# Optimization experiments

Measured on AMD Instinct MI355X. Metric: run time of the kernel, lower is better.

## Reference

```python
import jax, jax.numpy as jnp
import numpy as np

RES_W, RES_H = 256, 256
MAX_SAMPLES = 384
TF_RES = 128
FOV_DEG = 30.0
NEAR, FAR = 0.1, 100.0
BG = 0.0
HIT_EPS = 1e-3


def _normalize(v, axis=-1):
    return v / jnp.linalg.norm(v, axis=axis, keepdims=True)


def trilinear_sample(vol, tex):
    # vol: [X,Y,Z], tex: [...,3] in voxel coordinates
    res = np.array(vol.shape, dtype=np.float32)
    p = jnp.clip(tex, 0.0, jnp.asarray(res - 1.0 - 1e-6, jnp.float32))
    lo = jnp.floor(p).astype(jnp.int32)
    f = p - lo.astype(p.dtype)
    hi = jnp.minimum(lo + 1, jnp.asarray(res.astype(np.int32) - 1))
    x0, y0, z0 = lo[..., 0], lo[..., 1], lo[..., 2]
    x1, y1, z1 = hi[..., 0], hi[..., 1], hi[..., 2]
    fx, fy, fz = f[..., 0], f[..., 1], f[..., 2]
    c000 = vol[x0, y0, z0]; c100 = vol[x1, y0, z0]
    c010 = vol[x0, y1, z0]; c110 = vol[x1, y1, z0]
    c001 = vol[x0, y0, z1]; c101 = vol[x1, y0, z1]
    c011 = vol[x0, y1, z1]; c111 = vol[x1, y1, z1]
    c00 = c000 * (1 - fx) + c100 * fx
    c10 = c010 * (1 - fx) + c110 * fx
    c01 = c001 * (1 - fx) + c101 * fx
    c11 = c011 * (1 - fx) + c111 * fx
    c0 = c00 * (1 - fy) + c10 * fy
    c1 = c01 * (1 - fy) + c11 * fy
    return c0 * (1 - fz) + c1 * fz


def tf_lookup(tf, x):
    # tf: [T,4], x: [...] intensity in [0,1]
    T = tf.shape[0]
    xi = jnp.clip(x, 0.0, 1.0) * (T - 1)
    lo = jnp.floor(xi).astype(jnp.int32)
    hi = jnp.minimum(lo + 1, T - 1)
    f = (xi - lo.astype(xi.dtype))[..., None]
    return tf[lo] * (1 - f) + tf[hi] * f


def render_one(vol, tf, cam, sr):
    # vol [X,Y,Z], tf [T,4], cam [3] -> [W,H,5] (rgba + depth)
    W, H = RES_W, RES_H
    fwd = _normalize(-cam)
    world_up = jnp.array([0.0, 1.0, 0.0], jnp.float32)
    right = _normalize(jnp.cross(fwd, world_up))
    up = jnp.cross(right, fwd)
    tanf = jnp.tan(jnp.float32(np.radians(FOV_DEG) / 2))
    aspect = W / H
    u = ((jnp.arange(W) + 0.5) / W * 2 - 1) * tanf * aspect  # [W]
    v = ((jnp.arange(H) + 0.5) / H * 2 - 1) * tanf           # [H]
    dirs = fwd + u[:, None, None] * right + v[None, :, None] * up  # [W,H,3]
    dirs = _normalize(dirs)
    # ray-box intersection against [-1,1]^3
    inv = 1.0 / dirs
    t_lo = (-1.0 - cam) * inv
    t_hi = (1.0 - cam) * inv
    tmin = jnp.max(jnp.minimum(t_lo, t_hi), axis=-1)
    tmax = jnp.min(jnp.maximum(t_lo, t_hi), axis=-1)
    hit = (tmax >= 0.0) & (tmin <= tmax)
    entry = jnp.maximum(tmin, NEAR)
    dist = jnp.where(hit, jnp.maximum(tmax - entry, 0.0), 0.0)
    vol_max = max(vol.shape)
    # Nyquist: step = voxel size (2/vol_max) / sampling_rate
    ns = jnp.clip(jnp.ceil(dist * 0.5 * vol_max * sr), 1.0, MAX_SAMPLES)
    step = dist / ns
    k = jnp.arange(MAX_SAMPLES, dtype=jnp.float32)
    t = entry[..., None] + (k + 0.5) * step[..., None]            # [W,H,S]
    valid = (k < ns[..., None]) & hit[..., None]
    pos = cam + t[..., None] * dirs[..., None, :]                 # [W,H,S,3]
    res_m1 = jnp.asarray(np.array(vol.shape, np.float32) - 1.0)
    tex = (pos * 0.5 + 0.5) * res_m1
    intensity = trilinear_sample(vol, tex)                        # [W,H,S]
    rgba = tf_lookup(tf, intensity)                               # [W,H,S,4]
    a = rgba[..., 3]
    a = 1.0 - (1.0 - a) ** (1.0 / sr)   # opacity correction for sampling rate
    a = jnp.where(valid, a, 0.0)
    one_m = 1.0 - a
    cp = jnp.cumprod(one_m, axis=-1)
    T_excl = jnp.concatenate([jnp.ones_like(cp[..., :1]), cp[..., :-1]], axis=-1)
    w = T_excl * a                                                # [W,H,S]
    rgb = jnp.einsum('whs,whsc->whc', w, rgba[..., :3])
    acc = jnp.sum(w, axis=-1)
    rgb_out = rgb + (1.0 - acc)[..., None] * BG
    # FirstHitDepth
    hit_s = a > HIT_EPS
    any_hit = jnp.any(hit_s, axis=-1)
    first = jnp.argmax(hit_s, axis=-1)
    t_first = jnp.take_along_axis(t, first[..., None], axis=-1)[..., 0]
    depth = jnp.where(any_hit, (t_first - NEAR) / (FAR - NEAR), 1.0)
    return jnp.concatenate([rgb_out, acc[..., None], depth[..., None]], axis=-1)


def setup_inputs() -> dict:
    key = jax.random.key(0)
    k1, k2, k3 = jax.random.split(key, 3)
    volume = jax.random.uniform(k1, (1, 256, 256, 256), dtype=jnp.float32)
    tf = jax.random.uniform(k2, (1, TF_RES, 4), dtype=jnp.float32)
    look_from = jnp.array([[0.9, 0.7, -2.2]], jnp.float32) + 0.1 * jax.random.normal(k3, (1, 3), dtype=jnp.float32)
    return {"volume": volume, "tf": tf, "look_from": look_from, "sampling_rate": 1}


def reference(volume, tf, look_from, sampling_rate):
    sr = float(sampling_rate)
    return jax.vmap(lambda v, t, c: render_one(v, t, c, sr))(volume, tf, look_from)
```

## Files before the change

### kernel.cpp

```cpp
#include <hip/hip_runtime.h>
#include <math.h>

#define RES_W 256
#define RES_H 256
#define MAX_SAMPLES 384
#define TF_RES 128

__global__ __launch_bounds__(64) void raycast_kernel(
    const float* __restrict__ vol,
    const float* __restrict__ tf,
    const float* __restrict__ cam_p,
    const int*   __restrict__ sr_p,
    float* __restrict__ out)
{
    #pragma clang fp contract(off)

    __shared__ float4 tf_s[TF_RES];
    const int tid = threadIdx.y * 8 + threadIdx.x;
    const float4* tf4 = (const float4*)tf;
    tf_s[tid]      = tf4[tid];
    tf_s[tid + 64] = tf4[tid + 64];
    __syncthreads();

    const int h = blockIdx.x * 8 + threadIdx.x;
    const int w = blockIdx.y * 8 + threadIdx.y;

    const float cx = cam_p[0], cy = cam_p[1], cz = cam_p[2];
    const int   sr_i = sr_p[0];
    const float srf = (float)sr_i;

    float nx = -cx, ny = -cy, nz = -cz;
    float fl = __fsqrt_rn((nx*nx + ny*ny) + nz*nz);
    float fx = nx / fl, fy = ny / fl, fz = nz / fl;
    float rxu = 0.0f - fz;
    float rzu = fx;
    float rl = __fsqrt_rn((rxu*rxu + 0.0f) + rzu*rzu);
    float rx = rxu / rl, rz = rzu / rl;
    float ux = 0.0f - rz*fy;
    float uy = rz*fx - rx*fz;
    float uz = rx*fy;

    const float ang32 = (float)((30.0 * 0.017453292519943295) * 0.5);
    const float tan_half = (float)tan((double)ang32);

    float uu = ((((float)w + 0.5f) / 256.0f) * 2.0f - 1.0f) * tan_half;
    float vv = ((((float)h + 0.5f) / 256.0f) * 2.0f - 1.0f) * tan_half;

    float dx = (fx + uu*rx) + vv*ux;
    float dy = (fy + 0.0f ) + vv*uy;
    float dz = (fz + uu*rz) + vv*uz;
    float dl = __fsqrt_rn((dx*dx + dy*dy) + dz*dz);
    dx = dx / dl; dy = dy / dl; dz = dz / dl;

    float ivx = 1.0f/dx, ivy = 1.0f/dy, ivz = 1.0f/dz;
    float tlx = (-1.0f - cx)*ivx, thx = (1.0f - cx)*ivx;
    float tly = (-1.0f - cy)*ivy, thy = (1.0f - cy)*ivy;
    float tlz = (-1.0f - cz)*ivz, thz = (1.0f - cz)*ivz;
    float tmin = fmaxf(fmaxf(fminf(tlx,thx), fminf(tly,thy)), fminf(tlz,thz));
    float tmax = fminf(fminf(fmaxf(tlx,thx), fmaxf(tly,thy)), fmaxf(tlz,thz));
    bool hit = (tmax >= 0.0f) && (tmin <= tmax);

    float entry = fmaxf(tmin, 0.1f);
    float dist  = hit ? fmaxf(tmax - entry, 0.0f) : 0.0f;
    float nsf   = fminf(fmaxf(ceilf(((dist * 0.5f) * 256.0f) * srf), 1.0f), 384.0f);
    int   ns    = (int)nsf;
    float step  = dist / nsf;

    float rgb_r = 0.0f, rgb_g = 0.0f, rgb_b = 0.0f;
    float acc = 0.0f;
    float Texcl = 1.0f;
    float depth = 1.0f;
    bool  found = false;

    if (hit) {
        for (int k = 0; k < ns; ++k) {
            float t  = entry + ((float)k + 0.5f) * step;
            float px = (cx + t*dx);
            float py = (cy + t*dy);
            float pz = (cz + t*dz);
            px = ((px * 0.5f) + 0.5f) * 255.0f;
            py = ((py * 0.5f) + 0.5f) * 255.0f;
            pz = ((pz * 0.5f) + 0.5f) * 255.0f;
            px = fminf(fmaxf(px, 0.0f), 255.0f);
            py = fminf(fmaxf(py, 0.0f), 255.0f);
            pz = fminf(fmaxf(pz, 0.0f), 255.0f);
            int x0 = (int)floorf(px), y0 = (int)floorf(py), z0 = (int)floorf(pz);
            float ffx = px - (float)x0;
            float ffy = py - (float)y0;
            float ffz = pz - (float)z0;
            int x1 = min(x0 + 1, 255);
            int y1 = min(y0 + 1, 255);
            int z1 = min(z0 + 1, 255);

            int bx0 = x0 << 16, bx1 = x1 << 16;
            int by0 = y0 << 8,  by1 = y1 << 8;
            float c000 = vol[bx0 + by0 + z0];
            float c100 = vol[bx1 + by0 + z0];
            float c010 = vol[bx0 + by1 + z0];
            float c110 = vol[bx1 + by1 + z0];
            float c001 = vol[bx0 + by0 + z1];
            float c101 = vol[bx1 + by0 + z1];
            float c011 = vol[bx0 + by1 + z1];
            float c111 = vol[bx1 + by1 + z1];

            float omx = 1.0f - ffx, omy = 1.0f - ffy, omz = 1.0f - ffz;
            float c00 = c000*omx + c100*ffx;
            float c10 = c010*omx + c110*ffx;
            float c01 = c001*omx + c101*ffx;
            float c11 = c011*omx + c111*ffx;
            float c0  = c00*omy + c10*ffy;
            float c1  = c01*omy + c11*ffy;
            float intensity = c0*omz + c1*ffz;

            float xi = fminf(fmaxf(intensity, 0.0f), 1.0f) * 127.0f;
            int lo  = (int)floorf(xi);
            int hi2 = min(lo + 1, 127);
            float tfr = xi - (float)lo;
            float omt = 1.0f - tfr;
            float4 ca = tf_s[lo];
            float4 cb = tf_s[hi2];
            float cr  = ca.x*omt + cb.x*tfr;
            float cg  = ca.y*omt + cb.y*tfr;
            float cbb = ca.z*omt + cb.z*tfr;
            float a   = ca.w*omt + cb.w*tfr;

            if (sr_i == 1) {
                a = 1.0f - (1.0f - a);
            } else {
                a = 1.0f - powf(1.0f - a, 1.0f / srf);
            }

            float one_m = 1.0f - a;
            float wgt = Texcl * a;
            rgb_r += wgt * cr;
            rgb_g += wgt * cg;
            rgb_b += wgt * cbb;
            acc   += wgt;
            if (!found && a > 1e-3f) {
                found = true;
                depth = (t - 0.1f) / 99.9f;
            }
            Texcl = Texcl * one_m;
            if (found && Texcl < 1e-7f) break;
        }
    }

    {
        int oi = (w * RES_H + h) * 5;
        out[oi + 0] = rgb_r;
        out[oi + 1] = rgb_g;
        out[oi + 2] = rgb_b;
        out[oi + 3] = acc;
        out[oi + 4] = depth;
    }
}

extern "C" void kernel_launch(void* const* d_in, const int* in_sizes, int n_in,
                              void* d_out, int out_size, void* d_ws, size_t ws_size,
                              hipStream_t stream) {
    const float* vol = (const float*)d_in[0];
    const float* tf  = (const float*)d_in[1];
    const float* cam = (const float*)d_in[2];
    const int*   sr  = (const int*)d_in[3];
    float* out = (float*)d_out;

    dim3 block(8, 8, 1);
    dim3 grid(RES_H / 8, RES_W / 8, 1);
    raycast_kernel<<<grid, block, 0, stream>>>(vol, tf, cam, sr, out);
}
```

Baseline: 117.0 us.

## Batch four ray samples per iteration and remap block order across XCDs

The sample loop now computes positions and issues the gathers for four samples up front, then interpolates all four and composites them in order. This exposes more independent memory loads per thread to hide gather latency, at the cost of more registers and up to three wasted samples after early termination. The launch becomes a 1D grid whose block index is permuted so that spatially adjacent tiles land on the same chiplet, aiming to improve L2 locality for the volume reads.

```diff
diff --git a/kernel.cpp b/kernel.cpp
--- a/kernel.cpp
+++ b/kernel.cpp
@@ -16,14 +16,18 @@
     #pragma clang fp contract(off)
 
     __shared__ float4 tf_s[TF_RES];
-    const int tid = threadIdx.y * 8 + threadIdx.x;
+    const int tid = (int)threadIdx.x;
     const float4* tf4 = (const float4*)tf;
     tf_s[tid]      = tf4[tid];
     tf_s[tid + 64] = tf4[tid + 64];
     __syncthreads();
 
-    const int h = blockIdx.x * 8 + threadIdx.x;
-    const int w = blockIdx.y * 8 + threadIdx.y;
+    const int b    = (int)blockIdx.x;
+    const int tile = (b % 8) * 128 + (b / 8);
+    const int tile_h = tile % 32;
+    const int tile_w = tile / 32;
+    const int h = tile_h * 8 + (tid % 8);
+    const int w = tile_w * 8 + (tid / 8);
 
     const float cx = cam_p[0], cy = cam_p[1], cz = cam_p[2];
     const int   sr_i = sr_p[0];
@@ -73,74 +77,85 @@
     bool  found = false;
 
     if (hit) {
-        for (int k = 0; k < ns; ++k) {
-            float t  = entry + ((float)k + 0.5f) * step;
-            float px = (cx + t*dx);
-            float py = (cy + t*dy);
-            float pz = (cz + t*dz);
-            px = ((px * 0.5f) + 0.5f) * 255.0f;
-            py = ((py * 0.5f) + 0.5f) * 255.0f;
-            pz = ((pz * 0.5f) + 0.5f) * 255.0f;
-            px = fminf(fmaxf(px, 0.0f), 255.0f);
-            py = fminf(fmaxf(py, 0.0f), 255.0f);
-            pz = fminf(fmaxf(pz, 0.0f), 255.0f);
-            int x0 = (int)floorf(px), y0 = (int)floorf(py), z0 = (int)floorf(pz);
-            float ffx = px - (float)x0;
-            float ffy = py - (float)y0;
-            float ffz = pz - (float)z0;
-            int x1 = min(x0 + 1, 255);
-            int y1 = min(y0 + 1, 255);
-            int z1 = min(z0 + 1, 255);
-
-            int bx0 = x0 << 16, bx1 = x1 << 16;
-            int by0 = y0 << 8,  by1 = y1 << 8;
-            float c000 = vol[bx0 + by0 + z0];
-            float c100 = vol[bx1 + by0 + z0];
-            float c010 = vol[bx0 + by1 + z0];
-            float c110 = vol[bx1 + by1 + z0];
-            float c001 = vol[bx0 + by0 + z1];
-            float c101 = vol[bx1 + by0 + z1];
-            float c011 = vol[bx0 + by1 + z1];
-            float c111 = vol[bx1 + by1 + z1];
-
-            float omx = 1.0f - ffx, omy = 1.0f - ffy, omz = 1.0f - ffz;
-            float c00 = c000*omx + c100*ffx;
-            float c10 = c010*omx + c110*ffx;
-            float c01 = c001*omx + c101*ffx;
-            float c11 = c011*omx + c111*ffx;
-            float c0  = c00*omy + c10*ffy;
-            float c1  = c01*omy + c11*ffy;
-            float intensity = c0*omz + c1*ffz;
-
-            float xi = fminf(fmaxf(intensity, 0.0f), 1.0f) * 127.0f;
-            int lo  = (int)floorf(xi);
-            int hi2 = min(lo + 1, 127);
-            float tfr = xi - (float)lo;
-            float omt = 1.0f - tfr;
-            float4 ca = tf_s[lo];
-            float4 cb = tf_s[hi2];
-            float cr  = ca.x*omt + cb.x*tfr;
-            float cg  = ca.y*omt + cb.y*tfr;
-            float cbb = ca.z*omt + cb.z*tfr;
-            float a   = ca.w*omt + cb.w*tfr;
-
-            if (sr_i == 1) {
-                a = 1.0f - (1.0f - a);
-            } else {
-                a = 1.0f - powf(1.0f - a, 1.0f / srf);
+        for (int k0 = 0; k0 < ns; k0 += 4) {
+            float t_[4], val[4][8], ffx_[4], ffy_[4], ffz_[4];
+            #pragma unroll
+            for (int j = 0; j < 4; ++j) {
+                float t  = entry + ((float)(k0 + j) + 0.5f) * step;
+                t_[j] = t;
+                float px = (cx + t*dx);
+                float py = (cy + t*dy);
+                float pz = (cz + t*dz);
+                px = ((px * 0.5f) + 0.5f) * 255.0f;
+                py = ((py * 0.5f) + 0.5f) * 255.0f;
+                pz = ((pz * 0.5f) + 0.5f) * 255.0f;
+                px = fminf(fmaxf(px, 0.0f), 255.0f);
+                py = fminf(fmaxf(py, 0.0f), 255.0f);
+                pz = fminf(fmaxf(pz, 0.0f), 255.0f);
+                int x0 = (int)floorf(px), y0 = (int)floorf(py), z0 = (int)floorf(pz);
+                ffx_[j] = px - (float)x0;
+                ffy_[j] = py - (float)y0;
+                ffz_[j] = pz - (float)z0;
+                int x1 = min(x0 + 1, 255);
+                int y1 = min(y0 + 1, 255);
+                int z1 = min(z0 + 1, 255);
+                int bx0 = x0 << 16, bx1 = x1 << 16;
+                int by0 = y0 << 8,  by1 = y1 << 8;
+                val[j][0] = vol[bx0 + by0 + z0];
+                val[j][1] = vol[bx1 + by0 + z0];
+                val[j][2] = vol[bx0 + by1 + z0];
+                val[j][3] = vol[bx1 + by1 + z0];
+                val[j][4] = vol[bx0 + by0 + z1];
+                val[j][5] = vol[bx1 + by0 + z1];
+                val[j][6] = vol[bx0 + by1 + z1];
+                val[j][7] = vol[bx1 + by1 + z1];
             }
-
-            float one_m = 1.0f - a;
-            float wgt = Texcl * a;
-            rgb_r += wgt * cr;
-            rgb_g += wgt * cg;
-            rgb_b += wgt * cbb;
-            acc   += wgt;
-            if (!found && a > 1e-3f) {
-                found = true;
-                depth = (t - 0.1f) / 99.9f;
+            float tfr_[4];
+            float4 ca_[4], cb_[4];
+            #pragma unroll
+            for (int j = 0; j < 4; ++j) {
+                float omx = 1.0f - ffx_[j], omy = 1.0f - ffy_[j], omz = 1.0f - ffz_[j];
+                float c00 = val[j][0]*omx + val[j][1]*ffx_[j];
+                float c10 = val[j][2]*omx + val[j][3]*ffx_[j];
+                float c01 = val[j][4]*omx + val[j][5]*ffx_[j];
+                float c11 = val[j][6]*omx + val[j][7]*ffx_[j];
+                float c0  = c00*omy + c10*ffy_[j];
+                float c1  = c01*omy + c11*ffy_[j];
+                float intensity = c0*omz + c1*ffz_[j];
+                float xi = fminf(fmaxf(intensity, 0.0f), 1.0f) * 127.0f;
+                int lo  = (int)floorf(xi);
+                int hi2 = min(lo + 1, 127);
+                tfr_[j] = xi - (float)lo;
+                ca_[j] = tf_s[lo];
+                cb_[j] = tf_s[hi2];
             }
-            Texcl = Texcl * one_m;
+            #pragma unroll
+            for (int j = 0; j < 4; ++j) {
+                if (k0 + j < ns) {
+                    float tfr = tfr_[j];
+                    float omt = 1.0f - tfr;
+                    float cr  = ca_[j].x*omt + cb_[j].x*tfr;
+                    float cg  = ca_[j].y*omt + cb_[j].y*tfr;
+                    float cbb = ca_[j].z*omt + cb_[j].z*tfr;
+                    float a   = ca_[j].w*omt + cb_[j].w*tfr;
+                    if (sr_i == 1) {
+                        a = 1.0f - (1.0f - a);
+                    } else {
+                        a = 1.0f - powf(1.0f - a, 1.0f / srf);
+                    }
+                    float one_m = 1.0f - a;
+                    float wgt = Texcl * a;
+                    rgb_r += wgt * cr;
+                    rgb_g += wgt * cg;
+                    rgb_b += wgt * cbb;
+                    acc   += wgt;
+                    if (!found && a > 1e-3f) {
+                        found = true;
+                        depth = (t_[j] - 0.1f) / 99.9f;
+                    }
+                    Texcl = Texcl * one_m;
+                }
+            }
             if (found && Texcl < 1e-7f) break;
         }
     }
@@ -164,7 +179,5 @@
     const int*   sr  = (const int*)d_in[3];
     float* out = (float*)d_out;
 
-    dim3 block(8, 8, 1);
-    dim3 grid(RES_H / 8, RES_W / 8, 1);
-    raycast_kernel<<<grid, block, 0, stream>>>(vol, tf, cam, sr, out);
+    raycast_kernel<<<dim3(1024), dim3(64), 0, stream>>>(vol, tf, cam, sr, out);
 }
```

After: 113.0 us. -3.4%, faster.

## Parallelize each ray across 32 lanes with scan-based compositing

Applied to the files above, without the earlier changes.

Each ray is now handled by 32 lanes that sample 32 consecutive steps at once. Transmittance comes from a warp shuffle prefix product, colour and alpha from shuffle reductions, and first-hit depth from a min-reduction. The transfer function moves to a structure-of-arrays layout in shared memory, and blocks are remapped with a swizzle. This exposes far more memory-level parallelism for the scattered volume fetches than one-thread-per-ray marching, at the cost of shuffle overhead, wasted samples past early termination within a 32-chunk, and slightly different float summation order.

```diff
diff --git a/kernel.cpp b/kernel.cpp
--- a/kernel.cpp
+++ b/kernel.cpp
@@ -3,10 +3,9 @@
 
 #define RES_W 256
 #define RES_H 256
-#define MAX_SAMPLES 384
 #define TF_RES 128
 
-__global__ __launch_bounds__(64) void raycast_kernel(
+__global__ __launch_bounds__(256, 8) void raycast_kernel(
     const float* __restrict__ vol,
     const float* __restrict__ tf,
     const float* __restrict__ cam_p,
@@ -15,15 +14,22 @@
 {
     #pragma clang fp contract(off)
 
-    __shared__ float4 tf_s[TF_RES];
-    const int tid = threadIdx.y * 8 + threadIdx.x;
-    const float4* tf4 = (const float4*)tf;
-    tf_s[tid]      = tf4[tid];
-    tf_s[tid + 64] = tf4[tid + 64];
+    __shared__ float tfR[TF_RES], tfG[TF_RES], tfB[TF_RES], tfA[TF_RES];
+    const int tid = (int)threadIdx.x;
+    if (tid < TF_RES) {
+        float4 e = ((const float4*)tf)[tid];
+        tfR[tid] = e.x; tfG[tid] = e.y; tfB[tid] = e.z; tfA[tid] = e.w;
+    }
     __syncthreads();
 
-    const int h = blockIdx.x * 8 + threadIdx.x;
-    const int w = blockIdx.y * 8 + threadIdx.y;
+    const int lane = tid & 63;
+    const int sub  = lane & 31;
+
+    const int b  = (int)blockIdx.x;
+    const int sb = (b & 7) * 1024 + (b >> 3);
+    const int ray = sb * 8 + (tid >> 5);
+    const int h = ray & 255;
+    const int w = ray >> 8;
 
     const float cx = cam_p[0], cy = cam_p[1], cz = cam_p[2];
     const int   sr_i = sr_p[0];
@@ -66,86 +72,108 @@
     int   ns    = (int)nsf;
     float step  = dist / nsf;
 
-    float rgb_r = 0.0f, rgb_g = 0.0f, rgb_b = 0.0f;
-    float acc = 0.0f;
-    float Texcl = 1.0f;
+    float rgb_r = 0.0f, rgb_g = 0.0f, rgb_b = 0.0f, acc = 0.0f;
+    float T_prev = 1.0f;
     float depth = 1.0f;
     bool  found = false;
 
-    if (hit) {
-        for (int k = 0; k < ns; ++k) {
-            float t  = entry + ((float)k + 0.5f) * step;
-            float px = (cx + t*dx);
-            float py = (cy + t*dy);
-            float pz = (cz + t*dz);
-            px = ((px * 0.5f) + 0.5f) * 255.0f;
-            py = ((py * 0.5f) + 0.5f) * 255.0f;
-            pz = ((pz * 0.5f) + 0.5f) * 255.0f;
-            px = fminf(fmaxf(px, 0.0f), 255.0f);
-            py = fminf(fmaxf(py, 0.0f), 255.0f);
-            pz = fminf(fmaxf(pz, 0.0f), 255.0f);
-            int x0 = (int)floorf(px), y0 = (int)floorf(py), z0 = (int)floorf(pz);
-            float ffx = px - (float)x0;
-            float ffy = py - (float)y0;
-            float ffz = pz - (float)z0;
-            int x1 = min(x0 + 1, 255);
-            int y1 = min(y0 + 1, 255);
-            int z1 = min(z0 + 1, 255);
+    for (int base = 0; ; ) {
+        const int  k     = base + sub;
+        const bool valid = hit && (k < ns);
 
-            int bx0 = x0 << 16, bx1 = x1 << 16;
-            int by0 = y0 << 8,  by1 = y1 << 8;
-            float c000 = vol[bx0 + by0 + z0];
-            float c100 = vol[bx1 + by0 + z0];
-            float c010 = vol[bx0 + by1 + z0];
-            float c110 = vol[bx1 + by1 + z0];
-            float c001 = vol[bx0 + by0 + z1];
-            float c101 = vol[bx1 + by0 + z1];
-            float c011 = vol[bx0 + by1 + z1];
-            float c111 = vol[bx1 + by1 + z1];
+        float t  = entry + ((float)k + 0.5f) * step;
+        float px = (cx + t*dx);
+        float py = (cy + t*dy);
+        float pz = (cz + t*dz);
+        px = ((px * 0.5f) + 0.5f) * 255.0f;
+        py = ((py * 0.5f) + 0.5f) * 255.0f;
+        pz = ((pz * 0.5f) + 0.5f) * 255.0f;
+        px = fminf(fmaxf(px, 0.0f), 255.0f);
+        py = fminf(fmaxf(py, 0.0f), 255.0f);
+        pz = fminf(fmaxf(pz, 0.0f), 255.0f);
+        int x0 = (int)floorf(px), y0 = (int)floorf(py), z0 = (int)floorf(pz);
+        float ffx = px - (float)x0;
+        float ffy = py - (float)y0;
+        float ffz = pz - (float)z0;
+        int x1 = min(x0 + 1, 255);
+        int y1 = min(y0 + 1, 255);
+        int z1 = min(z0 + 1, 255);
+        int bx0 = x0 << 16, bx1 = x1 << 16;
+        int by0 = y0 << 8,  by1 = y1 << 8;
+        float c000 = vol[bx0 + by0 + z0];
+        float c100 = vol[bx1 + by0 + z0];
+        float c010 = vol[bx0 + by1 + z0];
+        float c110 = vol[bx1 + by1 + z0];
+        float c001 = vol[bx0 + by0 + z1];
+        float c101 = vol[bx1 + by0 + z1];
+        float c011 = vol[bx0 + by1 + z1];
+        float c111 = vol[bx1 + by1 + z1];
 
-            float omx = 1.0f - ffx, omy = 1.0f - ffy, omz = 1.0f - ffz;
-            float c00 = c000*omx + c100*ffx;
-            float c10 = c010*omx + c110*ffx;
-            float c01 = c001*omx + c101*ffx;
-            float c11 = c011*omx + c111*ffx;
-            float c0  = c00*omy + c10*ffy;
-            float c1  = c01*omy + c11*ffy;
-            float intensity = c0*omz + c1*ffz;
+        float omx = 1.0f - ffx, omy = 1.0f - ffy, omz = 1.0f - ffz;
+        float c00 = c000*omx + c100*ffx;
+        float c10 = c010*omx + c110*ffx;
+        float c01 = c001*omx + c101*ffx;
+        float c11 = c011*omx + c111*ffx;
+        float c0  = c00*omy + c10*ffy;
+        float c1  = c01*omy + c11*ffy;
+        float intensity = c0*omz + c1*ffz;
 
-            float xi = fminf(fmaxf(intensity, 0.0f), 1.0f) * 127.0f;
-            int lo  = (int)floorf(xi);
-            int hi2 = min(lo + 1, 127);
-            float tfr = xi - (float)lo;
-            float omt = 1.0f - tfr;
-            float4 ca = tf_s[lo];
-            float4 cb = tf_s[hi2];
-            float cr  = ca.x*omt + cb.x*tfr;
-            float cg  = ca.y*omt + cb.y*tfr;
-            float cbb = ca.z*omt + cb.z*tfr;
-            float a   = ca.w*omt + cb.w*tfr;
+        float xi = fminf(fmaxf(intensity, 0.0f), 1.0f) * 127.0f;
+        int lo  = (int)floorf(xi);
+        int hi2 = min(lo + 1, 127);
+        float tfr = xi - (float)lo;
+        float omt = 1.0f - tfr;
+        float cr  = tfR[lo]*omt + tfR[hi2]*tfr;
+        float cg  = tfG[lo]*omt + tfG[hi2]*tfr;
+        float cbb = tfB[lo]*omt + tfB[hi2]*tfr;
+        float a   = tfA[lo]*omt + tfA[hi2]*tfr;
 
-            if (sr_i == 1) {
-                a = 1.0f - (1.0f - a);
-            } else {
-                a = 1.0f - powf(1.0f - a, 1.0f / srf);
-            }
+        if (sr_i == 1) {
+            a = 1.0f - (1.0f - a);
+        } else {
+            a = 1.0f - powf(1.0f - a, 1.0f / srf);
+        }
+        if (!valid) a = 0.0f;
+        float one_m = 1.0f - a;
 
-            float one_m = 1.0f - a;
-            float wgt = Texcl * a;
-            rgb_r += wgt * cr;
-            rgb_g += wgt * cg;
-            rgb_b += wgt * cbb;
-            acc   += wgt;
-            if (!found && a > 1e-3f) {
-                found = true;
-                depth = (t - 0.1f) / 99.9f;
-            }
-            Texcl = Texcl * one_m;
-            if (found && Texcl < 1e-7f) break;
+        float x = one_m;
+        #pragma unroll
+        for (int off = 1; off < 32; off <<= 1) {
+            float y = __shfl_up(x, off);
+            if (sub >= off) x *= y;
         }
+        float ex = __shfl_up(x, 1);
+        if (sub == 0) ex = 1.0f;
+
+        float wgt = (T_prev * ex) * a;
+        float pr = wgt * cr, pg = wgt * cg, pb = wgt * cbb, pa = wgt;
+        #pragma unroll
+        for (int m = 16; m >= 1; m >>= 1) {
+            pr += __shfl_xor(pr, m);
+            pg += __shfl_xor(pg, m);
+            pb += __shfl_xor(pb, m);
+            pa += __shfl_xor(pa, m);
+        }
+        rgb_r += pr; rgb_g += pg; rgb_b += pb; acc += pa;
+
+        int hk = (valid && (a > 1e-3f)) ? k : 0x7FFFFFFF;
+        #pragma unroll
+        for (int m = 16; m >= 1; m >>= 1) hk = min(hk, __shfl_xor(hk, m));
+        if (!found && hk != 0x7FFFFFFF) {
+            found = true;
+            float tfh = entry + ((float)hk + 0.5f) * step;
+            depth = (tfh - 0.1f) / 99.9f;
+        }
+
+        float Tc = __shfl(x, (lane & 32) | 31);
+        T_prev = T_prev * Tc;
+
+        base += 32;
+        bool active = hit && (base < ns) && (T_prev >= 1e-7f);
+        if (__ballot(active) == 0ULL) break;
     }
 
-    {
+    if (sub == 0) {
         int oi = (w * RES_H + h) * 5;
         out[oi + 0] = rgb_r;
         out[oi + 1] = rgb_g;
@@ -164,7 +192,5 @@
     const int*   sr  = (const int*)d_in[3];
     float* out = (float*)d_out;
 
-    dim3 block(8, 8, 1);
-    dim3 grid(RES_H / 8, RES_W / 8, 1);
-    raycast_kernel<<<grid, block, 0, stream>>>(vol, tf, cam, sr, out);
+    raycast_kernel<<<dim3(8192), dim3(256), 0, stream>>>(vol, tf, cam, sr, out);
 }
```

Result: no change. 116.5 us (-0.4%).
